# Optimization experiments

Hardware: AMD Instinct MI355X
Metric: run time of the kernel (lower is better)

## Reference

```python
import jax, jax.numpy as jnp
import numpy as np

B, N, C, K = 4, 1024, 384, 10


def _sqdist(a, b):
    # a: [B,P,3], b: [B,M,3] -> [B,P,M] squared euclidean distance
    d = (jnp.sum(a * a, -1)[:, :, None] + jnp.sum(b * b, -1)[:, None, :]
         - 2.0 * jnp.einsum('bpc,bmc->bpm', a, b))
    return jnp.maximum(d, 0.0)


def _gather(points, idx):
    # points: [B,M,C], idx: [B,...] int -> [B,...,C]  (index_points)
    return jax.vmap(lambda p, i: p[i])(points, idx)


def setup_inputs() -> dict:
    key = jax.random.key(0)
    ks = jax.random.split(key, 8)
    def lin(k_, fan_in, fan_out):
        return jax.random.normal(k_, (fan_in, fan_out), jnp.float32) * (1.0 / np.sqrt(fan_in))
    return {
        'q': jax.random.normal(ks[0], (B, N, C), jnp.float32),
        'q_pos': jax.random.normal(ks[1], (B, N, 3), jnp.float32),
        'Wv': lin(ks[2], C, C), 'bv': jnp.zeros((C,), jnp.float32),
        'W1': lin(ks[3], 2 * C, C), 'b1': jnp.zeros((C,), jnp.float32),
        'ln_g': jnp.ones((C,), jnp.float32), 'ln_b': jnp.zeros((C,), jnp.float32),
        'W2': lin(ks[4], C, 3),
        'Wk': lin(ks[5], 2 * C, C), 'bk': jnp.zeros((C,), jnp.float32),
    }


def reference(q, q_pos, Wv, bv, W1, b1, ln_g, ln_b, W2, Wk, bk):
    Bq, Nq, Cq = q.shape
    # 1) KNN of each query among all points (self-attn: v=q, v_pos=q_pos)
    d = _sqdist(q_pos, q_pos)                      # [B,N,N]
    _, idx = jax.lax.top_k(-d, K)                  # [B,N,K] (smallest distances)
    # 2) offset prediction from gathered projected features + query feature
    v_off = q @ Wv + bv                            # [B,N,C]
    off_local_v = _gather(v_off, idx)              # [B,N,K,C]
    qk = jnp.broadcast_to(q[:, :, None, :], (Bq, Nq, K, Cq))
    shift_feat = jnp.concatenate([off_local_v, qk], -1)  # [B,N,K,2C]
    h = shift_feat @ W1 + b1
    mu = jnp.mean(h, -1, keepdims=True)
    var = jnp.var(h, -1, keepdims=True)
    h = (h - mu) / jnp.sqrt(var + 1e-5) * ln_g + ln_b     # LayerNorm
    h = jax.nn.gelu(h, approximate=False)
    offset = jnp.tanh(h @ W2)                      # [B,N,K,3]
    # 3) deformed positions, scaled by half the local bbox extent
    local_v_pos = _gather(q_pos, idx)              # [B,N,K,3]
    scale = (local_v_pos.max(-2) - local_v_pos.min(-2))[:, :, None, :] * 0.5
    shift_pos = (local_v_pos + offset * scale).reshape(Bq, Nq * K, 3)
    # 4) three_nn + three_interpolate (inverse-squared-distance weights)
    d2 = _sqdist(shift_pos, q_pos)                 # [B,NK,N]
    negd, idx3 = jax.lax.top_k(-d2, 3)             # [B,NK,3]
    dist = -negd
    w = 1.0 / (dist + 1e-8)
    w = w / jnp.sum(w, -1, keepdims=True)
    feats3 = _gather(q, idx3)                      # [B,NK,3,C]
    interp = jnp.einsum('bpt,bptc->bpc', w, feats3).reshape(Bq, Nq, K, Cq)
    # 5) graph conv: concat(diff, q) -> Linear -> LeakyReLU(0.2) -> max over K
    feature = jnp.concatenate([interp - qk, qk], -1)      # [B,N,K,2C]
    out = jax.nn.leaky_relu(feature @ Wk + bk, negative_slope=0.2)
    return out.max(-2)                             # [B,N,C]
```

## Files before the change

### kernel.cpp

```cpp
#include <hip/hip_runtime.h>
#include <math.h>

#define BB 4
#define NN 1024
#define CC 384
#define KK 10
#define NKK (NN*KK)

typedef __attribute__((ext_vector_type(8))) short short8v;
typedef __attribute__((ext_vector_type(8))) unsigned short ushort8v;
typedef __attribute__((ext_vector_type(4))) float f32x4;

template <int NA>
__device__ __forceinline__ void wave_sum_arr(float* a) {
  #pragma unroll
  for (int off = 32; off > 0; off >>= 1) {
    float t[NA];
    #pragma unroll
    for (int u = 0; u < NA; ++u) t[u] = __shfl_xor(a[u], off, 64);
    #pragma unroll
    for (int u = 0; u < NA; ++u) a[u] += t[u];
  }
}

__device__ __forceinline__ unsigned short f2bf(float x) {
  unsigned int b = __float_as_uint(x);
  return (unsigned short)((b + 0x7fffu + ((b >> 16) & 1u)) >> 16);
}
__device__ __forceinline__ float bf2f(unsigned short h) {
  return __uint_as_float(((unsigned int)h) << 16);
}

#define NB_CVT  (BB * NN * CC / 1024)
#define NB_PB   (2 * CC * CC / 256)
#define NB_PREP (NB_CVT + NB_PB + 3)
__global__ __launch_bounds__(256) void prep_gemm_kernel(
    const float* __restrict__ q,
    const float* __restrict__ W1, const float* __restrict__ b1,
    const float* __restrict__ bv, const float* __restrict__ bk,
    const float* __restrict__ Wk, const float* __restrict__ Wv,
    unsigned short* __restrict__ qh, unsigned short* __restrict__ ql,
    unsigned short* __restrict__ Wt,
    float* __restrict__ bias_uv, float* __restrict__ bias_pb,
    float* __restrict__ M1p) {
  int blk = blockIdx.x;
  int tid = threadIdx.x;
  if (blk < NB_CVT) {
    int i = (blk * 256 + tid) * 4;
    float4 v = *reinterpret_cast<const float4*>(q + i);
    float x[4] = {v.x, v.y, v.z, v.w};
    #pragma unroll
    for (int j = 0; j < 4; ++j) {
      unsigned short h = f2bf(x[j]);
      qh[i + j] = h;
      ql[i + j] = f2bf(x[j] - bf2f(h));
    }
    return;
  }
  if (blk < NB_CVT + NB_PB) {
    int idx = (blk - NB_CVT) * 256 + tid;
    int n = idx / CC, k = idx % CC;
    float v;
    if (n < CC) v = Wk[(size_t)k * CC + n];
    else        v = Wk[(size_t)CC * CC + k * CC + (n - CC)] - Wk[(size_t)k * CC + (n - CC)];
    Wt[(size_t)n * CC + k] = f2bf(v);
    return;
  }
  if (blk < NB_PREP) {
    int j = (blk - NB_CVT - NB_PB) * 256 + tid;
    if (j >= 2 * CC) return;
    if (j < CC) { bias_uv[j] = 0.f; bias_pb[j] = 0.f; }
    else {
      int c = j - CC;
      float s = b1[c];
      for (int i = 0; i < CC; ++i) s += bv[i] * W1[i * CC + c];
      bias_uv[j] = s;
      bias_pb[j] = bk[c];
    }
    return;
  }
  {
    int r = blk - NB_PREP;
    int bx = r % 3, by = (r / 3) % 3, bz = r / 9;
    __shared__ float As[16][132];
    __shared__ float Bs[16][128];
    int tx = tid & 15, ty = tid >> 4;
    int row0 = by * 128, col0 = bx * 128;
    int k0 = bz * 48;
    float acc[8][8] = {};
    int arow = tid >> 2, akc = (tid & 3) << 2;
    int brow = tid >> 5, bcol = (tid & 31) << 2;
    for (int kt = k0; kt < k0 + 48; kt += 16) {
      #pragma unroll
      for (int h = 0; h < 2; ++h) {
        int rr = arow + 64 * h;
        float4 av = *reinterpret_cast<const float4*>(Wv + (size_t)(row0 + rr) * CC + kt + akc);
        As[akc + 0][rr] = av.x; As[akc + 1][rr] = av.y;
        As[akc + 2][rr] = av.z; As[akc + 3][rr] = av.w;
      }
      #pragma unroll
      for (int h = 0; h < 2; ++h) {
        int rr = brow + 8 * h;
        float4 bv4 = *reinterpret_cast<const float4*>(W1 + (size_t)(kt + rr) * CC + col0 + bcol);
        *reinterpret_cast<float4*>(&Bs[rr][bcol]) = bv4;
      }
      __syncthreads();
      #pragma unroll
      for (int kk = 0; kk < 16; ++kk) {
        float4 a0 = *reinterpret_cast<const float4*>(&As[kk][ty << 2]);
        float4 a1 = *reinterpret_cast<const float4*>(&As[kk][64 + (ty << 2)]);
        float4 b0 = *reinterpret_cast<const float4*>(&Bs[kk][tx << 2]);
        float4 b1 = *reinterpret_cast<const float4*>(&Bs[kk][64 + (tx << 2)]);
        float av_[8] = {a0.x, a0.y, a0.z, a0.w, a1.x, a1.y, a1.z, a1.w};
        float bv_[8] = {b0.x, b0.y, b0.z, b0.w, b1.x, b1.y, b1.z, b1.w};
        #pragma unroll
        for (int i = 0; i < 8; ++i)
          #pragma unroll
          for (int j = 0; j < 8; ++j) acc[i][j] += av_[i] * bv_[j];
      }
      __syncthreads();
    }
    float* Cz = M1p + (size_t)bz * CC * CC;
    #pragma unroll
    for (int i = 0; i < 8; ++i) {
      int row = row0 + (ty << 2) + (i & 3) + ((i & 4) << 4);
      if (row >= CC) continue;
      #pragma unroll
      for (int h = 0; h < 2; ++h) {
        int col = col0 + 64 * h + (tx << 2);
        if (col >= CC) continue;
        float4 rv;
        rv.x = acc[i][4 * h + 0]; rv.y = acc[i][4 * h + 1];
        rv.z = acc[i][4 * h + 2]; rv.w = acc[i][4 * h + 3];
        *reinterpret_cast<float4*>(Cz + (size_t)row * CC + col) = rv;
      }
    }
  }
}

__global__ void pack_uv_split_kernel(const float* __restrict__ M1p, const float* __restrict__ W1,
                                     unsigned short* __restrict__ Buvh,
                                     unsigned short* __restrict__ Buvl) {
  int idx = blockIdx.x * 256 + threadIdx.x;
  int k = idx / (2 * CC), n = idx % (2 * CC);
  float val;
  if (n < CC) {
    float s = 0.f;
    #pragma unroll
    for (int p = 0; p < 8; ++p) s += M1p[(size_t)p * CC * CC + (size_t)k * CC + n];
    val = s;
  } else {
    val = W1[(size_t)(CC + k) * CC + (n - CC)];
  }
  unsigned short h = f2bf(val);
  Buvh[(size_t)n * CC + k] = h;
  Buvl[(size_t)n * CC + k] = f2bf(val - bf2f(h));
}

#define GEMM_NB 384
__global__ __launch_bounds__(256) void gemm_knn_kernel(
    const unsigned short* __restrict__ qh, const unsigned short* __restrict__ ql,
    const unsigned short* __restrict__ Buvh, const unsigned short* __restrict__ Buvl,
    const unsigned short* __restrict__ Wt,
    float* __restrict__ Cuv, float* __restrict__ Cpb,
    const float* __restrict__ bias_uv, const float* __restrict__ bias_pb,
    const float* __restrict__ q_pos, int* __restrict__ idxk, float* __restrict__ meta) {
  __shared__ __align__(16) char smem[32768];
  int blk = blockIdx.x;
  int tid = threadIdx.x;
  int lane = tid & 63, wave = tid >> 6;

  if (blk < GEMM_NB) {
    int path = blk / 192;
    int rem = blk % 192;
    int by = rem / 6, bx = rem % 6;
    unsigned short* Ah  = (unsigned short*)smem;
    unsigned short* Alo = (unsigned short*)(smem + 8192);
    unsigned short* Bhs = (unsigned short*)(smem + 16384);
    unsigned short* Bls = (unsigned short*)(smem + 24576);
    const unsigned short* Bh = path ? Wt : Buvh;
    float* Cm = path ? Cpb : Cuv;
    const float* bias = path ? bias_pb : bias_uv;
    int m0 = by * 128, n0 = bx * 128;
    f32x4 acc[4][4];
    #pragma unroll
    for (int i = 0; i < 4; ++i)
      #pragma unroll
      for (int j = 0; j < 4; ++j) acc[i][j] = (f32x4){0.f, 0.f, 0.f, 0.f};
    int rl = lane & 15, kg = lane >> 4;
    for (int k0 = 0; k0 < CC; k0 += 32) {
      #pragma unroll
      for (int j = 0; j < 2; ++j) {
        int id = tid + 256 * j;
        int r = id >> 2, s = id & 3;
        int sw = (s ^ (r & 3)) * 8;
        *reinterpret_cast<ushort8v*>(Ah + r * 32 + sw) =
            *reinterpret_cast<const ushort8v*>(qh + (size_t)(m0 + r) * CC + k0 + s * 8);
        *reinterpret_cast<ushort8v*>(Bhs + r * 32 + sw) =
            *reinterpret_cast<const ushort8v*>(Bh + (size_t)(n0 + r) * CC + k0 + s * 8);
        if (!path) {
          *reinterpret_cast<ushort8v*>(Alo + r * 32 + sw) =
              *reinterpret_cast<const ushort8v*>(ql + (size_t)(m0 + r) * CC + k0 + s * 8);
          *reinterpret_cast<ushort8v*>(Bls + r * 32 + sw) =
              *reinterpret_cast<const ushort8v*>(Buvl + (size_t)(n0 + r) * CC + k0 + s * 8);
        }
      }
      __syncthreads();
      short8v afh[4], bfh[4], afl[4], bfl[4];
      #pragma unroll
      for (int f = 0; f < 4; ++f) {
        int ar = (wave & 1) * 64 + f * 16 + rl;
        int aof = ar * 32 + (kg ^ (ar & 3)) * 8;
        int br = (wave >> 1) * 64 + f * 16 + rl;
        int bof = br * 32 + (kg ^ (br & 3)) * 8;
        afh[f] = *reinterpret_cast<const short8v*>(Ah + aof);
        bfh[f] = *reinterpret_cast<const short8v*>(Bhs + bof);
        if (!path) {
          afl[f] = *reinterpret_cast<const short8v*>(Alo + aof);
          bfl[f] = *reinterpret_cast<const short8v*>(Bls + bof);
        }
      }
      #pragma unroll
      for (int i = 0; i < 4; ++i) {
        #pragma unroll
        for (int j = 0; j < 4; ++j) {
          acc[i][j] = __builtin_amdgcn_mfma_f32_16x16x32_bf16(afh[i], bfh[j], acc[i][j], 0, 0, 0);
          if (!path) {
            acc[i][j] = __builtin_amdgcn_mfma_f32_16x16x32_bf16(afh[i], bfl[j], acc[i][j], 0, 0, 0);
            acc[i][j] = __builtin_amdgcn_mfma_f32_16x16x32_bf16(afl[i], bfh[j], acc[i][j], 0, 0, 0);
          }
        }
      }
      __syncthreads();
    }
    #pragma unroll
    for (int i = 0; i < 4; ++i) {
      #pragma unroll
      for (int j = 0; j < 4; ++j) {
        int col = n0 + (wave >> 1) * 64 + j * 16 + rl;
        float bcol_v = bias[col];
        #pragma unroll
        for (int r = 0; r < 4; ++r) {
          int row = m0 + (wave & 1) * 64 + i * 16 + kg * 4 + r;
          Cm[(size_t)row * (2 * CC) + col] = acc[i][j][r] + bcol_v;
        }
      }
    }
    return;
  }

  {
    int kblk = blk - GEMM_NB;
    int b = kblk >> 8;
    int ng = kblk & 255;
    int n = ng * 4 + wave;
    int bn = b * NN + n;
    float4* sp4 = (float4*)smem;

    const float* qp = q_pos + (size_t)b * NN * 3;
    for (int i = tid; i < NN; i += 256) {
      float x = qp[i * 3 + 0], y = qp[i * 3 + 1], z = qp[i * 3 + 2];
      sp4[i] = (float4){x, y, z, x * x + y * y + z * z};
    }
    __syncthreads();

    int nb[KK];
    {
      float4 me = sp4[n];
      float px = me.x, py = me.y, pz = me.z, sp = me.w;
      float bd[KK]; int bi[KK];
      #pragma unroll
      for (int s = 0; s < KK; ++s) { bd[s] = 1e30f; bi[s] = -1; }
      #pragma unroll 4
      for (int j = 0; j < 16; ++j) {
        int m = lane + (j << 6);
        float4 c = sp4[m];
        float dot = fmaf(px, c.x, fmaf(py, c.y, pz * c.z));
        float d = fmaf(-2.f, dot, sp + c.w);
        d = fmaxf(d, 0.f);
        if (d < bd[KK - 1]) {
          bd[KK - 1] = d; bi[KK - 1] = m;
          #pragma unroll
          for (int s = KK - 1; s >= 1; --s) {
            if (bd[s] < bd[s - 1]) {
              float td = bd[s]; bd[s] = bd[s - 1]; bd[s - 1] = td;
              int ti = bi[s]; bi[s] = bi[s - 1]; bi[s - 1] = ti;
            }
          }
        }
      }
      #pragma unroll
      for (int s = 0; s < KK; ++s) {
        float d = bd[0]; int i = bi[0];
        #pragma unroll
        for (int off = 32; off > 0; off >>= 1) {
          float od = __shfl_xor(d, off, 64);
          int oi = __shfl_xor(i, off, 64);
          if (od < d || (od == d && oi < i)) { d = od; i = oi; }
        }
        if (bi[0] == i) {
          #pragma unroll
          for (int u = 0; u < KK - 1; ++u) { bd[u] = bd[u + 1]; bi[u] = bi[u + 1]; }
          bd[KK - 1] = 1e30f; bi[KK - 1] = -1;
        }
        nb[s] = i;
      }
    }

    float sclx, scly, sclz;
    {
      float mxx = -1e30f, mnx = 1e30f, mxy = -1e30f, mny = 1e30f, mxz = -1e30f, mnz = 1e30f;
      #pragma unroll
      for (int k2 = 0; k2 < KK; ++k2) {
        float4 c = sp4[nb[k2]];
        mxx = fmaxf(mxx, c.x); mnx = fminf(mnx, c.x);
        mxy = fmaxf(mxy, c.y); mny = fminf(mny, c.y);
        mxz = fmaxf(mxz, c.z); mnz = fminf(mnz, c.z);
      }
      sclx = (mxx - mnx) * 0.5f; scly = (mxy - mny) * 0.5f; sclz = (mxz - mnz) * 0.5f;
    }

    int myn = 0;
    #pragma unroll
    for (int k = 0; k < KK; ++k) if (lane == k) myn = nb[k];
    float* mrow = meta + (size_t)bn * 36;
    if (lane < KK) {
      idxk[(size_t)bn * KK + lane] = myn;
      float4 c = sp4[myn];
      mrow[lane * 3 + 0] = c.x;
      mrow[lane * 3 + 1] = c.y;
      mrow[lane * 3 + 2] = c.z;
    }
    if (lane == 0) { mrow[30] = sclx; mrow[31] = scly; mrow[32] = sclz; }
  }
}

__global__ __launch_bounds__(256) void mlp_kernel(
    const float* __restrict__ Cat_uv, const float* __restrict__ lng, const float* __restrict__ lnb,
    const float* __restrict__ W2, const int* __restrict__ idxk, const float* __restrict__ meta,
    float* __restrict__ shp) {
  int tid = threadIdx.x;
  int wave = tid >> 6, lane = tid & 63;
  int bn = blockIdx.x * 2 + (wave >> 1);
  int b = bn >> 10;
  int kb = (wave & 1) * 5;

  int nb5[5];
  #pragma unroll
  for (int kk = 0; kk < 5; ++kk) nb5[kk] = idxk[(size_t)bn * KK + kb + kk];

  float Vv[6], lg[6], lb[6], w2a[6], w2b[6], w2c[6];
  const float* Vrow = Cat_uv + (size_t)bn * (2 * CC) + CC;
  #pragma unroll
  for (int i = 0; i < 6; ++i) {
    int c = lane + (i << 6);
    Vv[i] = Vrow[c];
    lg[i] = lng[c]; lb[i] = lnb[c];
    w2a[i] = W2[c * 3 + 0]; w2b[i] = W2[c * 3 + 1]; w2c[i] = W2[c * 3 + 2];
  }

  float hk[5][6];
  float sum[5];
  #pragma unroll
  for (int kk = 0; kk < 5; ++kk) {
    const float* Urow = Cat_uv + ((size_t)b * NN + nb5[kk]) * (2 * CC);
    float s = 0.f;
    #pragma unroll
    for (int i = 0; i < 6; ++i) {
      hk[kk][i] = Urow[lane + (i << 6)] + Vv[i];
      s += hk[kk][i];
    }
    sum[kk] = s;
  }
  wave_sum_arr<5>(sum);
  float mu[5], var[5];
  #pragma unroll
  for (int kk = 0; kk < 5; ++kk) {
    mu[kk] = sum[kk] * (1.0f / CC);
    float v = 0.f;
    #pragma unroll
    for (int i = 0; i < 6; ++i) { float d = hk[kk][i] - mu[kk]; v += d * d; }
    var[kk] = v;
  }
  wave_sum_arr<5>(var);
  float o[15];
  #pragma unroll
  for (int kk = 0; kk < 5; ++kk) {
    float rstd = 1.0f / sqrtf(var[kk] * (1.0f / CC) + 1e-5f);
    float o0 = 0.f, o1 = 0.f, o2 = 0.f;
    #pragma unroll
    for (int i = 0; i < 6; ++i) {
      float x = (hk[kk][i] - mu[kk]) * rstd * lg[i] + lb[i];
      float g = 0.5f * x * (1.0f + erff(x * 0.70710678118654752440f));
      o0 = fmaf(g, w2a[i], o0); o1 = fmaf(g, w2b[i], o1); o2 = fmaf(g, w2c[i], o2);
    }
    o[kk * 3 + 0] = o0; o[kk * 3 + 1] = o1; o[kk * 3 + 2] = o2;
  }
  wave_sum_arr<15>(o);
  float ox = 0.f, oy = 0.f, oz = 0.f;
  #pragma unroll
  for (int kk = 0; kk < 5; ++kk) {
    if (lane == kb + kk) { ox = o[kk * 3 + 0]; oy = o[kk * 3 + 1]; oz = o[kk * 3 + 2]; }
  }
  if (lane >= kb && lane < kb + 5) {
    const float* mrow = meta + (size_t)bn * 36;
    float lvx = mrow[lane * 3 + 0], lvy = mrow[lane * 3 + 1], lvz = mrow[lane * 3 + 2];
    float sclx = mrow[30], scly = mrow[31], sclz = mrow[32];
    float* sp = shp + ((size_t)bn * KK + lane) * 3;
    sp[0] = lvx + tanhf(ox) * sclx;
    sp[1] = lvy + tanhf(oy) * scly;
    sp[2] = lvz + tanhf(oz) * sclz;
  }
}

__global__ __launch_bounds__(256) void interp_kernel(
    const float* __restrict__ Cat_pb, const float* __restrict__ q_pos,
    const float* __restrict__ shp, float* __restrict__ out) {
  int bn = blockIdx.x;
  int b = bn >> 10;
  int tid = threadIdx.x;
  int wave = tid >> 6, lane = tid & 63;
  __shared__ float4 sp4[NN];
  __shared__ float s_shp[KK * 3];
  __shared__ float s_w[KK][3];
  __shared__ int s_i[KK][3];

  const float* qp = q_pos + (size_t)b * NN * 3;
  for (int i = tid; i < NN; i += 256) {
    float x = qp[i * 3 + 0], y = qp[i * 3 + 1], z = qp[i * 3 + 2];
    sp4[i] = (float4){x, y, z, x * x + y * y + z * z};
  }
  if (tid < KK * 3) s_shp[tid] = shp[(size_t)bn * KK * 3 + tid];
  __syncthreads();

  int cnt = (wave < 2) ? 3 : 2;
  int pbase = (wave < 2) ? wave * 3 : 6 + (wave - 2) * 2;
  float px[3], py[3], pz[3], ps[3];
  #pragma unroll
  for (int j = 0; j < 3; ++j) {
    int p = pbase + (j < cnt ? j : cnt - 1);
    px[j] = s_shp[p * 3 + 0]; py[j] = s_shp[p * 3 + 1]; pz[j] = s_shp[p * 3 + 2];
    ps[j] = fmaf(px[j], px[j], fmaf(py[j], py[j], pz[j] * pz[j]));
  }
  float d0[3], d1[3], d2[3]; int i0[3], i1[3], i2[3];
  #pragma unroll
  for (int j = 0; j < 3; ++j) { d0[j] = d1[j] = d2[j] = 1e30f; i0[j] = i1[j] = i2[j] = -1; }
  #pragma unroll 4
  for (int it = 0; it < 16; ++it) {
    int m = lane + (it << 6);
    float4 c = sp4[m];
    #pragma unroll
    for (int j = 0; j < 3; ++j) {
      float dot = fmaf(px[j], c.x, fmaf(py[j], c.y, pz[j] * c.z));
      float d = fmaf(-2.f, dot, ps[j] + c.w);
      d = fmaxf(d, 0.f);
      bool c2 = d < d2[j], c1 = d < d1[j], c0 = d < d0[j];
      d2[j] = c1 ? d1[j] : (c2 ? d : d2[j]);  i2[j] = c1 ? i1[j] : (c2 ? m : i2[j]);
      d1[j] = c0 ? d0[j] : (c1 ? d : d1[j]);  i1[j] = c0 ? i0[j] : (c1 ? m : i1[j]);
      d0[j] = c0 ? d : d0[j];                 i0[j] = c0 ? m : i0[j];
    }
  }
  float wd[3][3]; int wi[3][3];
  #pragma unroll
  for (int s = 0; s < 3; ++s) {
    float d[3]; int ii[3];
    #pragma unroll
    for (int j = 0; j < 3; ++j) { d[j] = d0[j]; ii[j] = i0[j]; }
    #pragma unroll
    for (int off = 32; off > 0; off >>= 1) {
      #pragma unroll
      for (int j = 0; j < 3; ++j) {
        float od = __shfl_xor(d[j], off, 64);
        int oi = __shfl_xor(ii[j], off, 64);
        if (od < d[j] || (od == d[j] && oi < ii[j])) { d[j] = od; ii[j] = oi; }
      }
    }
    #pragma unroll
    for (int j = 0; j < 3; ++j) {
      if (i0[j] == ii[j]) {
        d0[j] = d1[j]; i0[j] = i1[j]; d1[j] = d2[j]; i1[j] = i2[j]; d2[j] = 1e30f; i2[j] = -1;
      }
      wd[s][j] = d[j]; wi[s][j] = ii[j];
    }
  }
  if (lane == 0) {
    #pragma unroll
    for (int j = 0; j < 3; ++j) {
      if (j < cnt) {
        float w0 = 1.f / (wd[0][j] + 1e-8f), w1 = 1.f / (wd[1][j] + 1e-8f), w2 = 1.f / (wd[2][j] + 1e-8f);
        float s = w0 + w1 + w2;
        int p = pbase + j;
        s_w[p][0] = w0 / s; s_w[p][1] = w1 / s; s_w[p][2] = w2 / s;
        s_i[p][0] = wi[0][j]; s_i[p][1] = wi[1][j]; s_i[p][2] = wi[2][j];
      }
    }
  }
  __syncthreads();

  const float* Pb = Cat_pb + (size_t)b * NN * (2 * CC);
  const float* BseRow = Cat_pb + (size_t)bn * (2 * CC) + CC;
  for (int c = tid; c < CC; c += 256) {
    float base = BseRow[c];
    float best = -1e30f;
    #pragma unroll
    for (int k = 0; k < KK; ++k) {
      float acc = base;
      #pragma unroll
      for (int tt = 0; tt < 3; ++tt)
        acc = fmaf(s_w[k][tt], Pb[(size_t)s_i[k][tt] * (2 * CC) + c], acc);
      acc = acc >= 0.f ? acc : 0.2f * acc;
      best = fmaxf(best, acc);
    }
    out[(size_t)bn * CC + c] = best;
  }
}

extern "C" void kernel_launch(void* const* d_in, const int* in_sizes, int n_in,
                              void* d_out, int out_size, void* d_ws, size_t ws_size,
                              hipStream_t stream) {
  (void)in_sizes; (void)n_in; (void)out_size; (void)ws_size;
  const float* q    = (const float*)d_in[0];
  const float* qpos = (const float*)d_in[1];
  const float* Wv   = (const float*)d_in[2];
  const float* bv   = (const float*)d_in[3];
  const float* W1   = (const float*)d_in[4];
  const float* b1   = (const float*)d_in[5];
  const float* lng  = (const float*)d_in[6];
  const float* lnb  = (const float*)d_in[7];
  const float* W2   = (const float*)d_in[8];
  const float* Wk   = (const float*)d_in[9];
  const float* bk   = (const float*)d_in[10];
  float* out = (float*)d_out;

  float* ws = (float*)d_ws;
  float* Cat_uv = ws; ws += (size_t)BB * NN * 2 * CC;
  float* Cat_pb = ws; ws += (size_t)BB * NN * 2 * CC;
  float* M1p = Cat_pb;
  float* bias_uv = ws; ws += 2 * CC;
  float* bias_pb = ws; ws += 2 * CC;
  float* shp = ws; ws += (size_t)BB * NKK * 3;
  float* meta = ws; ws += (size_t)BB * NN * 36;
  unsigned short* qh = (unsigned short*)ws;  ws += (size_t)BB * NN * CC / 2;
  unsigned short* ql = (unsigned short*)ws;  ws += (size_t)BB * NN * CC / 2;
  unsigned short* Wt = (unsigned short*)ws;  ws += (size_t)2 * CC * CC / 2;
  unsigned short* Buvh = (unsigned short*)ws; ws += (size_t)2 * CC * CC / 2;
  unsigned short* Buvl = (unsigned short*)ws; ws += (size_t)2 * CC * CC / 2;
  int* idxk = (int*)ws;

  prep_gemm_kernel<<<dim3(NB_PREP + 72), dim3(256), 0, stream>>>(
      q, W1, b1, bv, bk, Wk, Wv, qh, ql, Wt, bias_uv, bias_pb, M1p);
  pack_uv_split_kernel<<<dim3(CC * 2 * CC / 256), dim3(256), 0, stream>>>(M1p, W1, Buvh, Buvl);
  gemm_knn_kernel<<<dim3(GEMM_NB + BB * NN / 4), dim3(256), 0, stream>>>(
      qh, ql, Buvh, Buvl, Wt, Cat_uv, Cat_pb, bias_uv, bias_pb, qpos, idxk, meta);
  mlp_kernel<<<dim3(BB * NN / 2), dim3(256), 0, stream>>>(
      Cat_uv, lng, lnb, W2, idxk, meta, shp);
  interp_kernel<<<dim3(BB * NN), dim3(256), 0, stream>>>(
      Cat_pb, qpos, shp, out);
}
```

Before: 140.7 us.

## Fuse offset MLP into interpolation kernel with wave-specialized roles

Removes the separate mlp_kernel launch and the shifted-position global buffer. Inside interp_kernel, waves 0-1 compute the LayerNorm/GELU offset MLP for 5 neighbors each and write shifted positions to shared memory, while waves 2-3 load the query positions into shared memory. The three-NN scan is then split so waves 0-1 handle 2 points each and waves 2-3 handle 3, balancing the extra MLP work. This saves a launch and a global round trip, but it lengthens the pre-barrier phase of each block and may raise register pressure.

```diff
diff --git a/kernel.cpp b/kernel.cpp
--- a/kernel.cpp
+++ b/kernel.cpp
@@ -335,87 +335,65 @@
   }
 }
 
-__global__ __launch_bounds__(256) void mlp_kernel(
-    const float* __restrict__ Cat_uv, const float* __restrict__ lng, const float* __restrict__ lnb,
-    const float* __restrict__ W2, const int* __restrict__ idxk, const float* __restrict__ meta,
-    float* __restrict__ shp) {
-  int tid = threadIdx.x;
-  int wave = tid >> 6, lane = tid & 63;
-  int bn = blockIdx.x * 2 + (wave >> 1);
-  int b = bn >> 10;
-  int kb = (wave & 1) * 5;
-
-  int nb5[5];
+template <int C>
+__device__ __forceinline__ void three_nn_scan(
+    const float4* sp4, const float* s_shp, int pbase, int lane,
+    float (&owd)[3][3], int (&owi)[3][3]) {
+  float px[C], py[C], pz[C], ps[C];
   #pragma unroll
-  for (int kk = 0; kk < 5; ++kk) nb5[kk] = idxk[(size_t)bn * KK + kb + kk];
-
-  float Vv[6], lg[6], lb[6], w2a[6], w2b[6], w2c[6];
-  const float* Vrow = Cat_uv + (size_t)bn * (2 * CC) + CC;
+  for (int j = 0; j < C; ++j) {
+    int p = pbase + j;
+    px[j] = s_shp[p * 3 + 0]; py[j] = s_shp[p * 3 + 1]; pz[j] = s_shp[p * 3 + 2];
+    ps[j] = fmaf(px[j], px[j], fmaf(py[j], py[j], pz[j] * pz[j]));
+  }
+  float d0[C], d1[C], d2[C]; int i0[C], i1[C], i2[C];
   #pragma unroll
-  for (int i = 0; i < 6; ++i) {
-    int c = lane + (i << 6);
-    Vv[i] = Vrow[c];
-    lg[i] = lng[c]; lb[i] = lnb[c];
-    w2a[i] = W2[c * 3 + 0]; w2b[i] = W2[c * 3 + 1]; w2c[i] = W2[c * 3 + 2];
-  }
-
-  float hk[5][6];
-  float sum[5];
+  for (int j = 0; j < C; ++j) { d0[j] = d1[j] = d2[j] = 1e30f; i0[j] = i1[j] = i2[j] = -1; }
+  #pragma unroll 4
+  for (int it = 0; it < 16; ++it) {
+    int m = lane + (it << 6);
+    float4 c = sp4[m];
+    #pragma unroll
+    for (int j = 0; j < C; ++j) {
+      float dot = fmaf(px[j], c.x, fmaf(py[j], c.y, pz[j] * c.z));
+      float d = fmaf(-2.f, dot, ps[j] + c.w);
+      d = fmaxf(d, 0.f);
+      bool c2 = d < d2[j], c1 = d < d1[j], c0 = d < d0[j];
+      d2[j] = c1 ? d1[j] : (c2 ? d : d2[j]);  i2[j] = c1 ? i1[j] : (c2 ? m : i2[j]);
+      d1[j] = c0 ? d0[j] : (c1 ? d : d1[j]);  i1[j] = c0 ? i0[j] : (c1 ? m : i1[j]);
+      d0[j] = c0 ? d : d0[j];                 i0[j] = c0 ? m : i0[j];
+    }
+  }
   #pragma unroll
-  for (int kk = 0; kk < 5; ++kk) {
-    const float* Urow = Cat_uv + ((size_t)b * NN + nb5[kk]) * (2 * CC);
-    float s = 0.f;
-    #pragma unroll
-    for (int i = 0; i < 6; ++i) {
-      hk[kk][i] = Urow[lane + (i << 6)] + Vv[i];
-      s += hk[kk][i];
-    }
-    sum[kk] = s;
-  }
-  wave_sum_arr<5>(sum);
-  float mu[5], var[5];
-  #pragma unroll
-  for (int kk = 0; kk < 5; ++kk) {
-    mu[kk] = sum[kk] * (1.0f / CC);
-    float v = 0.f;
-    #pragma unroll
-    for (int i = 0; i < 6; ++i) { float d = hk[kk][i] - mu[kk]; v += d * d; }
-    var[kk] = v;
-  }
-  wave_sum_arr<5>(var);
-  float o[15];
-  #pragma unroll
-  for (int kk = 0; kk < 5; ++kk) {
-    float rstd = 1.0f / sqrtf(var[kk] * (1.0f / CC) + 1e-5f);
-    float o0 = 0.f, o1 = 0.f, o2 = 0.f;
-    #pragma unroll
-    for (int i = 0; i < 6; ++i) {
-      float x = (hk[kk][i] - mu[kk]) * rstd * lg[i] + lb[i];
-      float g = 0.5f * x * (1.0f + erff(x * 0.70710678118654752440f));
-      o0 = fmaf(g, w2a[i], o0); o1 = fmaf(g, w2b[i], o1); o2 = fmaf(g, w2c[i], o2);
-    }
-    o[kk * 3 + 0] = o0; o[kk * 3 + 1] = o1; o[kk * 3 + 2] = o2;
-  }
-  wave_sum_arr<15>(o);
-  float ox = 0.f, oy = 0.f, oz = 0.f;
-  #pragma unroll
-  for (int kk = 0; kk < 5; ++kk) {
-    if (lane == kb + kk) { ox = o[kk * 3 + 0]; oy = o[kk * 3 + 1]; oz = o[kk * 3 + 2]; }
-  }
-  if (lane >= kb && lane < kb + 5) {
-    const float* mrow = meta + (size_t)bn * 36;
-    float lvx = mrow[lane * 3 + 0], lvy = mrow[lane * 3 + 1], lvz = mrow[lane * 3 + 2];
-    float sclx = mrow[30], scly = mrow[31], sclz = mrow[32];
-    float* sp = shp + ((size_t)bn * KK + lane) * 3;
-    sp[0] = lvx + tanhf(ox) * sclx;
-    sp[1] = lvy + tanhf(oy) * scly;
-    sp[2] = lvz + tanhf(oz) * sclz;
+  for (int s = 0; s < 3; ++s) {
+    float d[C]; int ii[C];
+    #pragma unroll
+    for (int j = 0; j < C; ++j) { d[j] = d0[j]; ii[j] = i0[j]; }
+    #pragma unroll
+    for (int off = 32; off > 0; off >>= 1) {
+      #pragma unroll
+      for (int j = 0; j < C; ++j) {
+        float od = __shfl_xor(d[j], off, 64);
+        int oi = __shfl_xor(ii[j], off, 64);
+        if (od < d[j] || (od == d[j] && oi < ii[j])) { d[j] = od; ii[j] = oi; }
+      }
+    }
+    #pragma unroll
+    for (int j = 0; j < C; ++j) {
+      if (i0[j] == ii[j]) {
+        d0[j] = d1[j]; i0[j] = i1[j]; d1[j] = d2[j]; i1[j] = i2[j]; d2[j] = 1e30f; i2[j] = -1;
+      }
+      owd[s][j] = d[j]; owi[s][j] = ii[j];
+    }
   }
 }
 
 __global__ __launch_bounds__(256) void interp_kernel(
-    const float* __restrict__ Cat_pb, const float* __restrict__ q_pos,
-    const float* __restrict__ shp, float* __restrict__ out) {
+    const float* __restrict__ Cat_uv, const float* __restrict__ Cat_pb,
+    const float* __restrict__ lng, const float* __restrict__ lnb,
+    const float* __restrict__ W2, const float* __restrict__ q_pos,
+    const int* __restrict__ idxk, const float* __restrict__ meta,
+    float* __restrict__ out) {
   int bn = blockIdx.x;
   int b = bn >> 10;
   int tid = threadIdx.x;
@@ -425,63 +403,88 @@
   __shared__ float s_w[KK][3];
   __shared__ int s_i[KK][3];
 
-  const float* qp = q_pos + (size_t)b * NN * 3;
-  for (int i = tid; i < NN; i += 256) {
-    float x = qp[i * 3 + 0], y = qp[i * 3 + 1], z = qp[i * 3 + 2];
-    sp4[i] = (float4){x, y, z, x * x + y * y + z * z};
-  }
-  if (tid < KK * 3) s_shp[tid] = shp[(size_t)bn * KK * 3 + tid];
+  if (wave >= 2) {
+    const float* qp = q_pos + (size_t)b * NN * 3;
+    for (int i = tid - 128; i < NN; i += 128) {
+      float x = qp[i * 3 + 0], y = qp[i * 3 + 1], z = qp[i * 3 + 2];
+      sp4[i] = (float4){x, y, z, x * x + y * y + z * z};
+    }
+  } else {
+    int kb = wave * 5;
+    int nb5[5];
+    #pragma unroll
+    for (int kk = 0; kk < 5; ++kk) nb5[kk] = idxk[(size_t)bn * KK + kb + kk];
+    float Vv[6], lg[6], lb[6], w2a[6], w2b[6], w2c[6];
+    const float* Vrow = Cat_uv + (size_t)bn * (2 * CC) + CC;
+    #pragma unroll
+    for (int i = 0; i < 6; ++i) {
+      int c = lane + (i << 6);
+      Vv[i] = Vrow[c];
+      lg[i] = lng[c]; lb[i] = lnb[c];
+      w2a[i] = W2[c * 3 + 0]; w2b[i] = W2[c * 3 + 1]; w2c[i] = W2[c * 3 + 2];
+    }
+    float hk[5][6];
+    float sum[5];
+    #pragma unroll
+    for (int kk = 0; kk < 5; ++kk) {
+      const float* Urow = Cat_uv + ((size_t)b * NN + nb5[kk]) * (2 * CC);
+      float s = 0.f;
+      #pragma unroll
+      for (int i = 0; i < 6; ++i) {
+        hk[kk][i] = Urow[lane + (i << 6)] + Vv[i];
+        s += hk[kk][i];
+      }
+      sum[kk] = s;
+    }
+    wave_sum_arr<5>(sum);
+    float mu[5], var[5];
+    #pragma unroll
+    for (int kk = 0; kk < 5; ++kk) {
+      mu[kk] = sum[kk] * (1.0f / CC);
+      float v = 0.f;
+      #pragma unroll
+      for (int i = 0; i < 6; ++i) { float d = hk[kk][i] - mu[kk]; v += d * d; }
+      var[kk] = v;
+    }
+    wave_sum_arr<5>(var);
+    float o[15];
+    #pragma unroll
+    for (int kk = 0; kk < 5; ++kk) {
+      float rstd = 1.0f / sqrtf(var[kk] * (1.0f / CC) + 1e-5f);
+      float o0 = 0.f, o1 = 0.f, o2 = 0.f;
+      #pragma unroll
+      for (int i = 0; i < 6; ++i) {
+        float x = (hk[kk][i] - mu[kk]) * rstd * lg[i] + lb[i];
+        float g = 0.5f * x * (1.0f + erff(x * 0.70710678118654752440f));
+        o0 = fmaf(g, w2a[i], o0); o1 = fmaf(g, w2b[i], o1); o2 = fmaf(g, w2c[i], o2);
+      }
+      o[kk * 3 + 0] = o0; o[kk * 3 + 1] = o1; o[kk * 3 + 2] = o2;
+    }
+    wave_sum_arr<15>(o);
+    float ox = 0.f, oy = 0.f, oz = 0.f;
+    #pragma unroll
+    for (int kk = 0; kk < 5; ++kk) {
+      if (lane == kb + kk) { ox = o[kk * 3 + 0]; oy = o[kk * 3 + 1]; oz = o[kk * 3 + 2]; }
+    }
+    if (lane >= kb && lane < kb + 5) {
+      const float* mrow = meta + (size_t)bn * 36;
+      float lvx = mrow[lane * 3 + 0], lvy = mrow[lane * 3 + 1], lvz = mrow[lane * 3 + 2];
+      float sclx = mrow[30], scly = mrow[31], sclz = mrow[32];
+      s_shp[lane * 3 + 0] = lvx + tanhf(ox) * sclx;
+      s_shp[lane * 3 + 1] = lvy + tanhf(oy) * scly;
+      s_shp[lane * 3 + 2] = lvz + tanhf(oz) * sclz;
+    }
+  }
   __syncthreads();
 
-  int cnt = (wave < 2) ? 3 : 2;
-  int pbase = (wave < 2) ? wave * 3 : 6 + (wave - 2) * 2;
-  float px[3], py[3], pz[3], ps[3];
-  #pragma unroll
-  for (int j = 0; j < 3; ++j) {
-    int p = pbase + (j < cnt ? j : cnt - 1);
-    px[j] = s_shp[p * 3 + 0]; py[j] = s_shp[p * 3 + 1]; pz[j] = s_shp[p * 3 + 2];
-    ps[j] = fmaf(px[j], px[j], fmaf(py[j], py[j], pz[j] * pz[j]));
-  }
-  float d0[3], d1[3], d2[3]; int i0[3], i1[3], i2[3];
-  #pragma unroll
-  for (int j = 0; j < 3; ++j) { d0[j] = d1[j] = d2[j] = 1e30f; i0[j] = i1[j] = i2[j] = -1; }
-  #pragma unroll 4
-  for (int it = 0; it < 16; ++it) {
-    int m = lane + (it << 6);
-    float4 c = sp4[m];
-    #pragma unroll
-    for (int j = 0; j < 3; ++j) {
-      float dot = fmaf(px[j], c.x, fmaf(py[j], c.y, pz[j] * c.z));
-      float d = fmaf(-2.f, dot, ps[j] + c.w);
-      d = fmaxf(d, 0.f);
-      bool c2 = d < d2[j], c1 = d < d1[j], c0 = d < d0[j];
-      d2[j] = c1 ? d1[j] : (c2 ? d : d2[j]);  i2[j] = c1 ? i1[j] : (c2 ? m : i2[j]);
-      d1[j] = c0 ? d0[j] : (c1 ? d : d1[j]);  i1[j] = c0 ? i0[j] : (c1 ? m : i1[j]);
-      d0[j] = c0 ? d : d0[j];                 i0[j] = c0 ? m : i0[j];
-    }
-  }
   float wd[3][3]; int wi[3][3];
-  #pragma unroll
-  for (int s = 0; s < 3; ++s) {
-    float d[3]; int ii[3];
-    #pragma unroll
-    for (int j = 0; j < 3; ++j) { d[j] = d0[j]; ii[j] = i0[j]; }
-    #pragma unroll
-    for (int off = 32; off > 0; off >>= 1) {
-      #pragma unroll
-      for (int j = 0; j < 3; ++j) {
-        float od = __shfl_xor(d[j], off, 64);
-        int oi = __shfl_xor(ii[j], off, 64);
-        if (od < d[j] || (od == d[j] && oi < ii[j])) { d[j] = od; ii[j] = oi; }
-      }
-    }
-    #pragma unroll
-    for (int j = 0; j < 3; ++j) {
-      if (i0[j] == ii[j]) {
-        d0[j] = d1[j]; i0[j] = i1[j]; d1[j] = d2[j]; i1[j] = i2[j]; d2[j] = 1e30f; i2[j] = -1;
-      }
-      wd[s][j] = d[j]; wi[s][j] = ii[j];
-    }
+  int pbase, cnt;
+  if (wave < 2) {
+    pbase = wave * 2; cnt = 2;
+    three_nn_scan<2>(sp4, s_shp, pbase, lane, wd, wi);
+  } else {
+    pbase = 4 + (wave - 2) * 3; cnt = 3;
+    three_nn_scan<3>(sp4, s_shp, pbase, lane, wd, wi);
   }
   if (lane == 0) {
     #pragma unroll
@@ -538,7 +541,6 @@
   float* M1p = Cat_pb;
   float* bias_uv = ws; ws += 2 * CC;
   float* bias_pb = ws; ws += 2 * CC;
-  float* shp = ws; ws += (size_t)BB * NKK * 3;
   float* meta = ws; ws += (size_t)BB * NN * 36;
   unsigned short* qh = (unsigned short*)ws;  ws += (size_t)BB * NN * CC / 2;
   unsigned short* ql = (unsigned short*)ws;  ws += (size_t)BB * NN * CC / 2;
@@ -552,8 +554,6 @@
   pack_uv_split_kernel<<<dim3(CC * 2 * CC / 256), dim3(256), 0, stream>>>(M1p, W1, Buvh, Buvl);
   gemm_knn_kernel<<<dim3(GEMM_NB + BB * NN / 4), dim3(256), 0, stream>>>(
       qh, ql, Buvh, Buvl, Wt, Cat_uv, Cat_pb, bias_uv, bias_pb, qpos, idxk, meta);
-  mlp_kernel<<<dim3(BB * NN / 2), dim3(256), 0, stream>>>(
-      Cat_uv, lng, lnb, W2, idxk, meta, shp);
   interp_kernel<<<dim3(BB * NN), dim3(256), 0, stream>>>(
-      Cat_pb, qpos, shp, out);
-}
+      Cat_uv, Cat_pb, lng, lnb, W2, qpos, idxk, meta, out);
+}
```

New measurement: 157.1 us. 1.12x slower.
